# Optimization experiments

Hardware: AMD Instinct MI355X
Metric: run time of the kernel (lower is better)

The kernel has to match this reference:

```python
import jax, jax.numpy as jnp
import numpy as np

B, T, A, OBS = 4096, 32, 4, 115
H, K, ACT = 64, 8, 19
FEAT = 4 + 3 + 4 * A          # 23 structured features
IN_DIM = FEAT + ACT * A       # 99 with action one-hots


def setup_inputs() -> dict:
    key = jax.random.key(0)
    ks = jax.random.split(key, 16)
    s = lambda *sh: 1.0 / np.sqrt(sh[-1])
    inp = {
        "obs_seq": jax.random.normal(ks[0], (B, T, A, OBS), jnp.float32),
        "action_seq": jax.random.randint(ks[1], (B, T, A), 0, ACT, jnp.int32),
        # feature_proj: Linear(IN_DIM->H) + LayerNorm(H)
        "proj_W": jax.random.normal(ks[2], (H, IN_DIM), jnp.float32) * s(H, IN_DIM),
        "proj_b": jnp.zeros((H,), jnp.float32),
        "ln_g": jnp.ones((H,), jnp.float32),
        "ln_b": jnp.zeros((H,), jnp.float32),
        # 2-layer GRU
        "Wih0": jax.random.normal(ks[3], (3 * H, H), jnp.float32) * s(1, H),
        "Whh0": jax.random.normal(ks[4], (3 * H, H), jnp.float32) * s(1, H),
        "bih0": jnp.zeros((3 * H,), jnp.float32),
        "bhh0": jnp.zeros((3 * H,), jnp.float32),
        "Wih1": jax.random.normal(ks[5], (3 * H, H), jnp.float32) * s(1, H),
        "Whh1": jax.random.normal(ks[6], (3 * H, H), jnp.float32) * s(1, H),
        "bih1": jnp.zeros((3 * H,), jnp.float32),
        "bhh1": jnp.zeros((3 * H,), jnp.float32),
        # classifier MLP
        "cls_W1": jax.random.normal(ks[7], (H, H), jnp.float32) * s(H, H),
        "cls_b1": jnp.zeros((H,), jnp.float32),
        "cls_W2": jax.random.normal(ks[8], (K, H), jnp.float32) * s(K, H),
        "cls_b2": jnp.zeros((K,), jnp.float32),
    }
    return inp


def _extract_features(obs_seq, action_seq):
    b, t, a = obs_seq.shape[:3]
    # ball position from player 0's obs, and its finite-difference velocity
    ball_pos = obs_seq[:, :, 0, 88:90]                       # [B,T,2]
    ball_vel = jnp.concatenate(
        [jnp.zeros_like(ball_pos[:, :1]), ball_pos[:, 1:] - ball_pos[:, :-1]], axis=1)
    pos = obs_seq[..., 0:2]                                   # [B,T,A,2]
    pos_flat = pos.reshape(b, t, a * 2)
    centroid = pos.mean(axis=2)                               # [B,T,2]
    spread = jnp.sqrt(((pos - centroid[:, :, None]) ** 2).sum(-1).mean(2, keepdims=True) + 1e-6)
    # closest-teammate relative position: vectorized argmin over pairwise dists
    diff = pos[:, :, :, None, :] - pos[:, :, None, :, :]      # [B,T,A,A,2]
    d2 = (diff ** 2).sum(-1)                                  # [B,T,A,A]
    d2 = jnp.where(jnp.eye(a, dtype=bool), jnp.inf, d2)       # exclude self
    idx = jnp.argmin(d2, axis=-1)                             # [B,T,A]
    nearest = jnp.take_along_axis(pos, idx[..., None], axis=2)  # [B,T,A,2]
    closest_rel = (nearest - pos).reshape(b, t, a * 2)
    onehot = jax.nn.one_hot(action_seq, ACT, dtype=jnp.float32).reshape(b, t, a * ACT)
    return jnp.concatenate(
        [ball_pos, ball_vel, pos_flat, centroid, spread, closest_rel, onehot], axis=-1)


def _gru_layer(x_tbh, Wih, Whh, bih, bhh):
    h0 = jnp.zeros((x_tbh.shape[1], Whh.shape[1]), x_tbh.dtype)

    def step(h, x):
        gi = x @ Wih.T + bih
        gh = h @ Whh.T + bhh
        ir, iz, inn = jnp.split(gi, 3, axis=-1)
        hr, hz, hn = jnp.split(gh, 3, axis=-1)
        r = jax.nn.sigmoid(ir + hr)
        z = jax.nn.sigmoid(iz + hz)
        n = jnp.tanh(inn + r * hn)
        h_new = (1.0 - z) * n + z * h
        return h_new, h_new

    h_last, ys = jax.lax.scan(step, h0, x_tbh)
    return ys, h_last


def reference(obs_seq, action_seq, proj_W, proj_b, ln_g, ln_b,
              Wih0, Whh0, bih0, bhh0, Wih1, Whh1, bih1, bhh1,
              cls_W1, cls_b1, cls_W2, cls_b2):
    feats = _extract_features(obs_seq, action_seq)            # [B,T,99]
    x = feats @ proj_W.T + proj_b                             # [B,T,H]
    mu = x.mean(-1, keepdims=True)
    var = x.var(-1, keepdims=True)
    x = (x - mu) * jax.lax.rsqrt(var + 1e-5) * ln_g + ln_b
    x = jax.nn.relu(x)
    x = jnp.swapaxes(x, 0, 1)                                 # [T,B,H]
    ys0, _ = _gru_layer(x, Wih0, Whh0, bih0, bhh0)
    _, h_last = _gru_layer(ys0, Wih1, Whh1, bih1, bhh1)       # [B,H]
    hid = jax.nn.relu(h_last @ cls_W1.T + cls_b1)
    logits = hid @ cls_W2.T + cls_b2                          # [B,K]
    return logits
```

## Files before the change

### kernel.cpp

```cpp
#include <hip/hip_runtime.h>

#define B_ 4096
#define T_ 32
#define A_ 4
#define OBS_ 115
#define H_ 64
#define IN_DIM_ 99
#define ACT_ 19
#define NBT (B_*T_)

typedef _Float16 f16;
typedef _Float16 f16x8 __attribute__((ext_vector_type(8)));
typedef float f32x4 __attribute__((ext_vector_type(4)));

static __device__ __forceinline__ float sigmoid_f(float x) {
    return __builtin_amdgcn_rcpf(1.f + __expf(-x));
}
static __device__ __forceinline__ float tanh_f(float x) {
    return 1.f - 2.f * __builtin_amdgcn_rcpf(1.f + __expf(2.f * x));
}
static __device__ __forceinline__ f32x4 mfma16(f16x8 a, f16x8 b, f32x4 c) {
    return __builtin_amdgcn_mfma_f32_16x16x32_f16(a, b, c, 0, 0, 0);
}

__global__ __launch_bounds__(256) void k0_transpose(const float* __restrict__ W,
                                                    float* __restrict__ WT) {
    int idx = blockIdx.x * 256 + threadIdx.x;
    if (idx < IN_DIM_ * H_) {
        int i = idx >> 6, h = idx & 63;
        WT[idx] = W[h * IN_DIM_ + i];
    }
}

__global__ __launch_bounds__(256) void k1_fused(const float* __restrict__ obs,
                                                const int* __restrict__ act,
                                                const float* __restrict__ WT,
                                                const float* __restrict__ pb,
                                                const float* __restrict__ lng,
                                                const float* __restrict__ lnb,
                                                f16* __restrict__ xout) {
    __shared__ float fl[256 * 25];
    __shared__ int al[256 * 5];
    int tid = threadIdx.x;
    int n = blockIdx.x * 256 + tid;
    const float* o = obs + (size_t)n * (A_ * OBS_);

    float px[A_], py[A_];
#pragma unroll
    for (int a = 0; a < A_; a++) { px[a] = o[a * OBS_]; py[a] = o[a * OBS_ + 1]; }
    float bx = o[88], by = o[89];
    int t0 = n & (T_ - 1);
    float pbx = bx, pby = by;
    if (t0 > 0) { pbx = o[88 - A_ * OBS_]; pby = o[89 - A_ * OBS_]; }

    float cx = (px[0] + px[1] + px[2] + px[3]) * 0.25f;
    float cy = (py[0] + py[1] + py[2] + py[3]) * 0.25f;
    float sp = 0.f;
#pragma unroll
    for (int a = 0; a < A_; a++) { float dx = px[a] - cx, dy = py[a] - cy; sp += dx * dx + dy * dy; }
    sp = sqrtf(sp * 0.25f + 1e-6f);

    float crx[A_], cry[A_];
#pragma unroll
    for (int i = 0; i < A_; i++) {
        float best = 3.4e38f; int bj = 0;
#pragma unroll
        for (int j = 0; j < A_; j++) {
            if (j == i) continue;
            float dx = px[i] - px[j], dy = py[i] - py[j];
            float d2 = dx * dx + dy * dy;
            if (d2 < best) { best = d2; bj = j; }
        }
        crx[i] = px[bj] - px[i]; cry[i] = py[bj] - py[i];
    }

    float* f = &fl[tid * 25];
    f[0] = bx; f[1] = by; f[2] = bx - pbx; f[3] = by - pby;
#pragma unroll
    for (int a = 0; a < A_; a++) { f[4 + 2 * a] = px[a]; f[5 + 2 * a] = py[a]; }
    f[12] = cx; f[13] = cy; f[14] = sp;
#pragma unroll
    for (int a = 0; a < A_; a++) { f[15 + 2 * a] = crx[a]; f[16 + 2 * a] = cry[a]; }
#pragma unroll
    for (int a = 0; a < A_; a++) al[tid * 5 + a] = act[n * A_ + a];
    __syncthreads();

    int lane = tid & 63;
    int wv = __builtin_amdgcn_readfirstlane(tid >> 6);
    float wc[23];
#pragma unroll
    for (int i = 0; i < 23; i++) wc[i] = WT[i * 64 + lane];
    float pbv = pb[lane], g = lng[lane], bb = lnb[lane];
    int b0 = blockIdx.x * 8 + wv * 2;

    for (int it = 0; it < 64; it++) {
        int lb = wv * 64 + it;
        int b = b0 + (it >> 5);
        int t = it & 31;
        const float* fp = &fl[lb * 25];
        float v = pbv;
#pragma unroll
        for (int i = 0; i < 23; i++) v += fp[i] * wc[i];
#pragma unroll
        for (int a = 0; a < A_; a++) {
            int ai = al[lb * 5 + a];
            v += WT[(23 + a * ACT_ + ai) * 64 + lane];
        }
        float s = v, ss = v * v;
#pragma unroll
        for (int m = 1; m < 64; m <<= 1) {
            s += __shfl_xor(s, m, 64);
            ss += __shfl_xor(ss, m, 64);
        }
        float mean = s * (1.f / 64.f);
        float var = ss * (1.f / 64.f) - mean * mean;
        float xn = (v - mean) * rsqrtf(var + 1e-5f) * g + bb;
        xn = fmaxf(xn, 0.f);
        xout[((size_t)t * B_ + b) * 64 + lane] = (f16)xn;
    }
}

__global__ __launch_bounds__(256, 1) void k2_gru(
        const f16* __restrict__ x,
        const float* __restrict__ Wih0, const float* __restrict__ Whh0,
        const float* __restrict__ bih0, const float* __restrict__ bhh0,
        const float* __restrict__ Wih1, const float* __restrict__ Whh1,
        const float* __restrict__ bih1, const float* __restrict__ bhh1,
        const float* __restrict__ W1, const float* __restrict__ b1,
        const float* __restrict__ W2, const float* __restrict__ b2,
        float* __restrict__ out) {
    __shared__ __align__(16) f16 hbuf[2][2][16 * 72];
    int tid = threadIdx.x;
    int lane = tid & 63;
    int wv = __builtin_amdgcn_readfirstlane(tid >> 6);
    int c = lane & 15, q = lane >> 4;
    int S = wv * 16;
    int rowbase = blockIdx.x * 16;

    for (int k = tid; k < 2 * 2 * 16 * 72; k += 256) ((f16*)hbuf)[k] = (f16)0.f;

    auto ldw = [&](const float* W, int row0, int kcol) -> f16x8 {
        const float* p = W + (size_t)(row0 + c) * 64 + kcol + q * 8;
        f32x4 w0 = *(const f32x4*)p;
        f32x4 w1 = *(const f32x4*)(p + 4);
        f16x8 r;
        r[0] = (f16)w0[0]; r[1] = (f16)w0[1]; r[2] = (f16)w0[2]; r[3] = (f16)w0[3];
        r[4] = (f16)w1[0]; r[5] = (f16)w1[1]; r[6] = (f16)w1[2]; r[7] = (f16)w1[3];
        return r;
    };

    f16x8 wih0[3][2], whh0[3][2], wih1[3][2], whh1[3][2];
#pragma unroll
    for (int g = 0; g < 3; g++)
#pragma unroll
        for (int kf = 0; kf < 2; kf++) {
            wih0[g][kf] = ldw(Wih0, g * 64 + S, kf * 32);
            whh0[g][kf] = ldw(Whh0, g * 64 + S, kf * 32);
            wih1[g][kf] = ldw(Wih1, g * 64 + S, kf * 32);
            whh1[g][kf] = ldw(Whh1, g * 64 + S, kf * 32);
        }

    float br0 = bih0[S + c] + bhh0[S + c];
    float bz0 = bih0[64 + S + c] + bhh0[64 + S + c];
    float bi0 = bih0[128 + S + c];
    float bh0 = bhh0[128 + S + c];
    float br1 = bih1[S + c] + bhh1[S + c];
    float bz1 = bih1[64 + S + c] + bhh1[64 + S + c];
    float bi1 = bih1[128 + S + c];
    float bh1 = bhh1[128 + S + c];
    f32x4 vbr0 = {br0, br0, br0, br0}, vbz0 = {bz0, bz0, bz0, bz0};
    f32x4 vbi0 = {bi0, bi0, bi0, bi0}, vbh0 = {bh0, bh0, bh0, bh0};
    f32x4 vbr1 = {br1, br1, br1, br1}, vbz1 = {bz1, bz1, bz1, bz1};
    f32x4 vbi1 = {bi1, bi1, bi1, bi1}, vbh1 = {bh1, bh1, bh1, bh1};

    f32x4 h0c = {0.f, 0.f, 0.f, 0.f}, h1c = {0.f, 0.f, 0.f, 0.f};

    auto ldx = [&](int t, int kf) -> f16x8 {
        return *(const f16x8*)(x + ((size_t)t * B_ + rowbase + c) * 64 + kf * 32 + q * 8);
    };

    __syncthreads();

    int p = 0;
    f16x8 xa0 = ldx(0, 0), xa1 = ldx(0, 1);
    f16x8 xn0 = xa0, xn1 = xa1;

    for (int i = 0; i <= T_; i++) {
        if (i + 1 < T_) { xn0 = ldx(i + 1, 0); xn1 = ldx(i + 1, 1); }

        f16x8 a00 = *(const f16x8*)&hbuf[0][p][c * 72 + q * 8];
        f16x8 a01 = *(const f16x8*)&hbuf[0][p][c * 72 + 32 + q * 8];

        if (i < T_) {
            f32x4 r = vbr0, z = vbz0, in = vbi0, hn = vbh0;
            r = mfma16(a00, whh0[0][0], r); r = mfma16(a01, whh0[0][1], r);
            r = mfma16(xa0, wih0[0][0], r); r = mfma16(xa1, wih0[0][1], r);
            z = mfma16(a00, whh0[1][0], z); z = mfma16(a01, whh0[1][1], z);
            z = mfma16(xa0, wih0[1][0], z); z = mfma16(xa1, wih0[1][1], z);
            in = mfma16(xa0, wih0[2][0], in); in = mfma16(xa1, wih0[2][1], in);
            hn = mfma16(a00, whh0[2][0], hn); hn = mfma16(a01, whh0[2][1], hn);
#pragma unroll
            for (int rr = 0; rr < 4; rr++) {
                float rg = sigmoid_f(r[rr]);
                float zg = sigmoid_f(z[rr]);
                float ng = tanh_f(in[rr] + rg * hn[rr]);
                h0c[rr] = ng + zg * (h0c[rr] - ng);
            }
        }
        if (i > 0) {
            f16x8 a10 = *(const f16x8*)&hbuf[1][p][c * 72 + q * 8];
            f16x8 a11 = *(const f16x8*)&hbuf[1][p][c * 72 + 32 + q * 8];
            f32x4 r = vbr1, z = vbz1, in = vbi1, hn = vbh1;
            r = mfma16(a10, whh1[0][0], r); r = mfma16(a11, whh1[0][1], r);
            r = mfma16(a00, wih1[0][0], r); r = mfma16(a01, wih1[0][1], r);
            z = mfma16(a10, whh1[1][0], z); z = mfma16(a11, whh1[1][1], z);
            z = mfma16(a00, wih1[1][0], z); z = mfma16(a01, wih1[1][1], z);
            in = mfma16(a00, wih1[2][0], in); in = mfma16(a01, wih1[2][1], in);
            hn = mfma16(a10, whh1[2][0], hn); hn = mfma16(a11, whh1[2][1], hn);
#pragma unroll
            for (int rr = 0; rr < 4; rr++) {
                float rg = sigmoid_f(r[rr]);
                float zg = sigmoid_f(z[rr]);
                float ng = tanh_f(in[rr] + rg * hn[rr]);
                h1c[rr] = ng + zg * (h1c[rr] - ng);
            }
        }
#pragma unroll
        for (int rr = 0; rr < 4; rr++) {
            hbuf[0][p ^ 1][(q * 4 + rr) * 72 + S + c] = (f16)h0c[rr];
            hbuf[1][p ^ 1][(q * 4 + rr) * 72 + S + c] = (f16)h1c[rr];
        }
        __syncthreads();
        p ^= 1;
        xa0 = xn0; xa1 = xn1;
    }

    f16x8 ha0 = *(const f16x8*)&hbuf[1][p][c * 72 + q * 8];
    f16x8 ha1 = *(const f16x8*)&hbuf[1][p][c * 72 + 32 + q * 8];
    f16x8 w1f0 = ldw(W1, S, 0), w1f1 = ldw(W1, S, 32);
    float bw1 = b1[S + c];
    f32x4 hid = {bw1, bw1, bw1, bw1};
    hid = mfma16(ha0, w1f0, hid);
    hid = mfma16(ha1, w1f1, hid);
#pragma unroll
    for (int rr = 0; rr < 4; rr++) {
        float hv = fmaxf(hid[rr], 0.f);
        hbuf[0][p ^ 1][(q * 4 + rr) * 72 + S + c] = (f16)hv;
    }
    __syncthreads();
    if (wv == 0) {
        f16x8 ga0 = *(const f16x8*)&hbuf[0][p ^ 1][c * 72 + q * 8];
        f16x8 ga1 = *(const f16x8*)&hbuf[0][p ^ 1][c * 72 + 32 + q * 8];
        f16x8 w2f0 = {}, w2f1 = {};
        float bo = 0.f;
        if (c < 8) {
            w2f0 = ldw(W2, 0, 0);
            w2f1 = ldw(W2, 0, 32);
            bo = b2[c];
        }
        f32x4 lg = {bo, bo, bo, bo};
        lg = mfma16(ga0, w2f0, lg);
        lg = mfma16(ga1, w2f1, lg);
        if (c < 8) {
#pragma unroll
            for (int rr = 0; rr < 4; rr++)
                out[(size_t)(rowbase + q * 4 + rr) * 8 + c] = lg[rr];
        }
    }
}

extern "C" void kernel_launch(void* const* d_in, const int* in_sizes, int n_in,
                              void* d_out, int out_size, void* d_ws, size_t ws_size,
                              hipStream_t stream) {
    const float* obs  = (const float*)d_in[0];
    const int*   act  = (const int*)d_in[1];
    const float* projW = (const float*)d_in[2];
    const float* projb = (const float*)d_in[3];
    const float* lng  = (const float*)d_in[4];
    const float* lnb  = (const float*)d_in[5];
    const float* Wih0 = (const float*)d_in[6];
    const float* Whh0 = (const float*)d_in[7];
    const float* bih0 = (const float*)d_in[8];
    const float* bhh0 = (const float*)d_in[9];
    const float* Wih1 = (const float*)d_in[10];
    const float* Whh1 = (const float*)d_in[11];
    const float* bih1 = (const float*)d_in[12];
    const float* bhh1 = (const float*)d_in[13];
    const float* W1   = (const float*)d_in[14];
    const float* b1   = (const float*)d_in[15];
    const float* W2   = (const float*)d_in[16];
    const float* b2   = (const float*)d_in[17];
    float* out = (float*)d_out;

    char* ws = (char*)d_ws;
    float* WT = (float*)ws;
    f16*   xw = (f16*)(ws + 32768);

    k0_transpose<<<25, 256, 0, stream>>>(projW, WT);
    k1_fused<<<NBT / 256, 256, 0, stream>>>(obs, act, WT, projb, lng, lnb, xw);
    k2_gru<<<B_ / 16, 256, 0, stream>>>(xw, Wih0, Whh0, bih0, bhh0,
                                        Wih1, Whh1, bih1, bhh1,
                                        W1, b1, W2, b2, out);
}
```

Measured before the change: 392.1 us.

## Split GRU layers across separate wave groups with 512-thread blocks

Doubles the GRU block to 8 waves and gives layer 0 and layer 1 their own 4-wave groups, so each wave holds only one layer's weights and runs one layer's recurrence step per iteration. The two layers, already skewed by one timestep, now execute concurrently on different waves instead of serially in the same wave. This cuts per-wave register use and the serial per-step latency, but 256 blocks of 512 threads still leaves many CUs with one block.

New measurement: 394.9 us. No clear change (+0.7%).

```diff
diff --git a/kernel.cpp b/kernel.cpp
--- a/kernel.cpp
+++ b/kernel.cpp
@@ -120,7 +120,7 @@
     }
 }
 
-__global__ __launch_bounds__(256, 1) void k2_gru(
+__global__ __launch_bounds__(512, 1) void k2_gru(
         const f16* __restrict__ x,
         const float* __restrict__ Wih0, const float* __restrict__ Whh0,
         const float* __restrict__ bih0, const float* __restrict__ bhh0,
@@ -133,11 +133,12 @@
     int tid = threadIdx.x;
     int lane = tid & 63;
     int wv = __builtin_amdgcn_readfirstlane(tid >> 6);
+    int L = wv >> 2;
+    int S = (wv & 3) * 16;
     int c = lane & 15, q = lane >> 4;
-    int S = wv * 16;
     int rowbase = blockIdx.x * 16;
 
-    for (int k = tid; k < 2 * 2 * 16 * 72; k += 256) ((f16*)hbuf)[k] = (f16)0.f;
+    for (int k = tid; k < 2 * 2 * 16 * 72; k += 512) ((f16*)hbuf)[k] = (f16)0.f;
 
     auto ldw = [&](const float* W, int row0, int kcol) -> f16x8 {
         const float* p = W + (size_t)(row0 + c) * 64 + kcol + q * 8;
@@ -149,31 +150,28 @@
         return r;
     };
 
-    f16x8 wih0[3][2], whh0[3][2], wih1[3][2], whh1[3][2];
+    const float* Wih = L ? Wih1 : Wih0;
+    const float* Whh = L ? Whh1 : Whh0;
+    const float* bih = L ? bih1 : bih0;
+    const float* bhh = L ? bhh1 : bhh0;
+
+    f16x8 wih[3][2], whh[3][2];
 #pragma unroll
     for (int g = 0; g < 3; g++)
 #pragma unroll
         for (int kf = 0; kf < 2; kf++) {
-            wih0[g][kf] = ldw(Wih0, g * 64 + S, kf * 32);
-            whh0[g][kf] = ldw(Whh0, g * 64 + S, kf * 32);
-            wih1[g][kf] = ldw(Wih1, g * 64 + S, kf * 32);
-            whh1[g][kf] = ldw(Whh1, g * 64 + S, kf * 32);
-        }
-
-    float br0 = bih0[S + c] + bhh0[S + c];
-    float bz0 = bih0[64 + S + c] + bhh0[64 + S + c];
-    float bi0 = bih0[128 + S + c];
-    float bh0 = bhh0[128 + S + c];
-    float br1 = bih1[S + c] + bhh1[S + c];
-    float bz1 = bih1[64 + S + c] + bhh1[64 + S + c];
-    float bi1 = bih1[128 + S + c];
-    float bh1 = bhh1[128 + S + c];
-    f32x4 vbr0 = {br0, br0, br0, br0}, vbz0 = {bz0, bz0, bz0, bz0};
-    f32x4 vbi0 = {bi0, bi0, bi0, bi0}, vbh0 = {bh0, bh0, bh0, bh0};
-    f32x4 vbr1 = {br1, br1, br1, br1}, vbz1 = {bz1, bz1, bz1, bz1};
-    f32x4 vbi1 = {bi1, bi1, bi1, bi1}, vbh1 = {bh1, bh1, bh1, bh1};
-
-    f32x4 h0c = {0.f, 0.f, 0.f, 0.f}, h1c = {0.f, 0.f, 0.f, 0.f};
+            wih[g][kf] = ldw(Wih, g * 64 + S, kf * 32);
+            whh[g][kf] = ldw(Whh, g * 64 + S, kf * 32);
+        }
+
+    float br = bih[S + c] + bhh[S + c];
+    float bz = bih[64 + S + c] + bhh[64 + S + c];
+    float bi = bih[128 + S + c];
+    float bh = bhh[128 + S + c];
+    f32x4 vbr = {br, br, br, br}, vbz = {bz, bz, bz, bz};
+    f32x4 vbi = {bi, bi, bi, bi}, vbh = {bh, bh, bh, bh};
+
+    f32x4 hc = {0.f, 0.f, 0.f, 0.f};
 
     auto ldx = [&](int t, int kf) -> f16x8 {
         return *(const f16x8*)(x + ((size_t)t * B_ + rowbase + c) * 64 + kf * 32 + q * 8);
@@ -182,70 +180,60 @@
     __syncthreads();
 
     int p = 0;
-    f16x8 xa0 = ldx(0, 0), xa1 = ldx(0, 1);
-    f16x8 xn0 = xa0, xn1 = xa1;
+    f16x8 xa0 = {}, xa1 = {}, xn0 = {}, xn1 = {};
+    if (L == 0) { xa0 = ldx(0, 0); xa1 = ldx(0, 1); xn0 = xa0; xn1 = xa1; }
 
     for (int i = 0; i <= T_; i++) {
-        if (i + 1 < T_) { xn0 = ldx(i + 1, 0); xn1 = ldx(i + 1, 1); }
-
-        f16x8 a00 = *(const f16x8*)&hbuf[0][p][c * 72 + q * 8];
-        f16x8 a01 = *(const f16x8*)&hbuf[0][p][c * 72 + 32 + q * 8];
-
-        if (i < T_) {
-            f32x4 r = vbr0, z = vbz0, in = vbi0, hn = vbh0;
-            r = mfma16(a00, whh0[0][0], r); r = mfma16(a01, whh0[0][1], r);
-            r = mfma16(xa0, wih0[0][0], r); r = mfma16(xa1, wih0[0][1], r);
-            z = mfma16(a00, whh0[1][0], z); z = mfma16(a01, whh0[1][1], z);
-            z = mfma16(xa0, wih0[1][0], z); z = mfma16(xa1, wih0[1][1], z);
-            in = mfma16(xa0, wih0[2][0], in); in = mfma16(xa1, wih0[2][1], in);
-            hn = mfma16(a00, whh0[2][0], hn); hn = mfma16(a01, whh0[2][1], hn);
+        f16x8 hh0, hh1, in0, in1;
+        if (L == 0) {
+            if (i + 1 < T_) { xn0 = ldx(i + 1, 0); xn1 = ldx(i + 1, 1); }
+            hh0 = *(const f16x8*)&hbuf[0][p][c * 72 + q * 8];
+            hh1 = *(const f16x8*)&hbuf[0][p][c * 72 + 32 + q * 8];
+            in0 = xa0; in1 = xa1;
+        } else {
+            hh0 = *(const f16x8*)&hbuf[1][p][c * 72 + q * 8];
+            hh1 = *(const f16x8*)&hbuf[1][p][c * 72 + 32 + q * 8];
+            in0 = *(const f16x8*)&hbuf[0][p][c * 72 + q * 8];
+            in1 = *(const f16x8*)&hbuf[0][p][c * 72 + 32 + q * 8];
+        }
+        bool active = L ? (i > 0) : (i < T_);
+        if (active) {
+            f32x4 r = vbr, z = vbz, in_ = vbi, hn = vbh;
+            r = mfma16(hh0, whh[0][0], r); r = mfma16(hh1, whh[0][1], r);
+            r = mfma16(in0, wih[0][0], r); r = mfma16(in1, wih[0][1], r);
+            z = mfma16(hh0, whh[1][0], z); z = mfma16(hh1, whh[1][1], z);
+            z = mfma16(in0, wih[1][0], z); z = mfma16(in1, wih[1][1], z);
+            in_ = mfma16(in0, wih[2][0], in_); in_ = mfma16(in1, wih[2][1], in_);
+            hn = mfma16(hh0, whh[2][0], hn); hn = mfma16(hh1, whh[2][1], hn);
 #pragma unroll
             for (int rr = 0; rr < 4; rr++) {
                 float rg = sigmoid_f(r[rr]);
                 float zg = sigmoid_f(z[rr]);
-                float ng = tanh_f(in[rr] + rg * hn[rr]);
-                h0c[rr] = ng + zg * (h0c[rr] - ng);
+                float ng = tanh_f(in_[rr] + rg * hn[rr]);
+                hc[rr] = ng + zg * (hc[rr] - ng);
             }
         }
-        if (i > 0) {
-            f16x8 a10 = *(const f16x8*)&hbuf[1][p][c * 72 + q * 8];
-            f16x8 a11 = *(const f16x8*)&hbuf[1][p][c * 72 + 32 + q * 8];
-            f32x4 r = vbr1, z = vbz1, in = vbi1, hn = vbh1;
-            r = mfma16(a10, whh1[0][0], r); r = mfma16(a11, whh1[0][1], r);
-            r = mfma16(a00, wih1[0][0], r); r = mfma16(a01, wih1[0][1], r);
-            z = mfma16(a10, whh1[1][0], z); z = mfma16(a11, whh1[1][1], z);
-            z = mfma16(a00, wih1[1][0], z); z = mfma16(a01, wih1[1][1], z);
-            in = mfma16(a00, wih1[2][0], in); in = mfma16(a01, wih1[2][1], in);
-            hn = mfma16(a10, whh1[2][0], hn); hn = mfma16(a11, whh1[2][1], hn);
-#pragma unroll
-            for (int rr = 0; rr < 4; rr++) {
-                float rg = sigmoid_f(r[rr]);
-                float zg = sigmoid_f(z[rr]);
-                float ng = tanh_f(in[rr] + rg * hn[rr]);
-                h1c[rr] = ng + zg * (h1c[rr] - ng);
-            }
-        }
-#pragma unroll
-        for (int rr = 0; rr < 4; rr++) {
-            hbuf[0][p ^ 1][(q * 4 + rr) * 72 + S + c] = (f16)h0c[rr];
-            hbuf[1][p ^ 1][(q * 4 + rr) * 72 + S + c] = (f16)h1c[rr];
-        }
+#pragma unroll
+        for (int rr = 0; rr < 4; rr++)
+            hbuf[L][p ^ 1][(q * 4 + rr) * 72 + S + c] = (f16)hc[rr];
         __syncthreads();
         p ^= 1;
-        xa0 = xn0; xa1 = xn1;
+        if (L == 0) { xa0 = xn0; xa1 = xn1; }
     }
 
     f16x8 ha0 = *(const f16x8*)&hbuf[1][p][c * 72 + q * 8];
     f16x8 ha1 = *(const f16x8*)&hbuf[1][p][c * 72 + 32 + q * 8];
-    f16x8 w1f0 = ldw(W1, S, 0), w1f1 = ldw(W1, S, 32);
-    float bw1 = b1[S + c];
-    f32x4 hid = {bw1, bw1, bw1, bw1};
-    hid = mfma16(ha0, w1f0, hid);
-    hid = mfma16(ha1, w1f1, hid);
-#pragma unroll
-    for (int rr = 0; rr < 4; rr++) {
-        float hv = fmaxf(hid[rr], 0.f);
-        hbuf[0][p ^ 1][(q * 4 + rr) * 72 + S + c] = (f16)hv;
+    if (L == 0) {
+        f16x8 w1f0 = ldw(W1, S, 0), w1f1 = ldw(W1, S, 32);
+        float bw1 = b1[S + c];
+        f32x4 hid = {bw1, bw1, bw1, bw1};
+        hid = mfma16(ha0, w1f0, hid);
+        hid = mfma16(ha1, w1f1, hid);
+#pragma unroll
+        for (int rr = 0; rr < 4; rr++) {
+            float hv = fmaxf(hid[rr], 0.f);
+            hbuf[0][p ^ 1][(q * 4 + rr) * 72 + S + c] = (f16)hv;
+        }
     }
     __syncthreads();
     if (wv == 0) {
@@ -298,7 +286,7 @@
 
     k0_transpose<<<25, 256, 0, stream>>>(projW, WT);
     k1_fused<<<NBT / 256, 256, 0, stream>>>(obs, act, WT, projb, lng, lnb, xw);
-    k2_gru<<<B_ / 16, 256, 0, stream>>>(xw, Wih0, Whh0, bih0, bhh0,
+    k2_gru<<<B_ / 16, 512, 0, stream>>>(xw, Wih0, Whh0, bih0, bhh0,
                                         Wih1, Whh1, bih1, bhh1,
                                         W1, b1, W2, b2, out);
 }
```
